# Optimization experiments

Hardware: AMD Instinct MI355X
Metric: run time of the kernel (lower is better)

Reference implementation:

```python
import jax, jax.numpy as jnp
import numpy as np

K = 256  # number of leaf nodes in the cluster tree


def setup_inputs() -> dict:
    key = jax.random.key(0)
    k1, k2 = jax.random.split(key)
    minibatch = jax.random.normal(k1, (131072, 64), dtype=jnp.float32)
    centers = jax.random.normal(k2, (K, 64), dtype=jnp.float32)
    return {"minibatch": minibatch, "centers": centers}


def reference(minibatch, centers):
    # Euclidean cdist (p=2) between samples [N,D] and leaf centers [K,D]
    x_sq = jnp.sum(minibatch * minibatch, axis=1, keepdims=True)      # [N,1]
    c_sq = jnp.sum(centers * centers, axis=1)[None, :]                # [1,K]
    dist_sq = x_sq + c_sq - 2.0 * (minibatch @ centers.T)             # [N,K]
    dist_sq = jnp.maximum(dist_sq, 0.0)
    dist = jnp.sqrt(dist_sq)

    # nearest-leaf routing (torch.min over dim=1)
    assignments = jnp.argmin(dist, axis=1)                            # [N] int
    min_dists = jnp.min(dist, axis=1)                                 # [N]

    # per-leaf statistics (vectorized form of the per-node assignment loop):
    # counts -> node.assignments length, sums -> analytic center updates,
    # sum_sq -> node.sum_squared_dist
    ones = jnp.ones(minibatch.shape[0], dtype=minibatch.dtype)
    leaf_counts = jax.ops.segment_sum(ones, assignments, num_segments=K)           # [K]
    leaf_sums = jax.ops.segment_sum(minibatch, assignments, num_segments=K)        # [K,D]
    leaf_sum_sq_dist = jax.ops.segment_sum(min_dists * min_dists, assignments,
                                           num_segments=K)                         # [K]
    return assignments, min_dists, leaf_counts, leaf_sums, leaf_sum_sq_dist
```

## Files before the change

kernel.cpp:

```cpp
#include <hip/hip_runtime.h>
#include <hip/hip_bf16.h>
#include <float.h>

#define NS 131072
#define DD 64
#define KK 256
#define CPAD 72
#define NSTAT 16896
#define XTS 264
#define XTSW 132
#define NCOPY 512
#define RGROUPS 16
#define RPER 32
#define SCR_OFF_F ((size_t)NCOPY * NSTAT / 2)
#define P_OFF_F   (SCR_OFF_F + (size_t)RGROUPS * NSTAT)
#define P_CSQ_F 9216
#define P_IMG_I4 2304

typedef __attribute__((ext_vector_type(8))) short bf16x8;
typedef __attribute__((ext_vector_type(4))) float f32x4;
typedef __attribute__((ext_vector_type(4))) unsigned int u32x4;


__global__ void zero_buf(float* __restrict__ p, int n) {
    int i = blockIdx.x * 256 + threadIdx.x;
    if (i < n) p[i] = 0.f;
}

__device__ inline unsigned short f2bf(float f) {
    union { __hip_bfloat16 h; unsigned short u; } v;
    v.h = __float2bfloat16(f);
    return v.u;
}
__device__ inline float bf2f(unsigned short b) {
    return __uint_as_float(((unsigned)b) << 16);
}

__global__ void prep_centers(const float* __restrict__ ctr, float* __restrict__ P) {
    __shared__ float s_part[32][9];
    const int t = threadIdx.x;
    const int rl = t >> 3, seg = t & 7;
    const int r = blockIdx.x * 32 + rl;
    const float* rp = ctr + r * DD + seg * 8;
    float4 a = ((const float4*)rp)[0];
    float4 b = ((const float4*)rp)[1];
    unsigned short u0 = f2bf(a.x), u1 = f2bf(a.y), u2 = f2bf(a.z), u3 = f2bf(a.w);
    unsigned short u4 = f2bf(b.x), u5 = f2bf(b.y), u6 = f2bf(b.z), u7 = f2bf(b.w);
    float q0 = bf2f(u0), q1 = bf2f(u1), q2 = bf2f(u2), q3 = bf2f(u3);
    float q4 = bf2f(u4), q5 = bf2f(u5), q6 = bf2f(u6), q7 = bf2f(u7);
    float p = (q0*q0 + q1*q1 + q2*q2 + q3*q3) + (q4*q4 + q5*q5 + q6*q6 + q7*q7);

    unsigned short* Pu = (unsigned short*)P;
    int4 pack;
    pack.x = (int)((unsigned)u0 | ((unsigned)u1 << 16));
    pack.y = (int)((unsigned)u2 | ((unsigned)u3 << 16));
    pack.z = (int)((unsigned)u4 | ((unsigned)u5 << 16));
    pack.w = (int)((unsigned)u6 | ((unsigned)u7 << 16));
    *(int4*)(Pu + (size_t)r * CPAD + seg * 8) = pack;
    if (seg == 0) {
        int4 z; z.x = 0; z.y = 0; z.z = 0; z.w = 0;
        *(int4*)(Pu + (size_t)r * CPAD + 64) = z;
    }
    s_part[rl][seg] = p;
    __syncthreads();
    if (seg == 0) {
        float s = 0.f;
        #pragma unroll
        for (int k = 0; k < 8; ++k) s += s_part[rl][k];
        P[P_CSQ_F + r] = s;
    }
}

__global__ __launch_bounds__(256, 4)
void deepect_argmin(const float* __restrict__ mb, const float* __restrict__ P,
                    float* __restrict__ out) {
    __shared__ __align__(16) unsigned short s_ctr[KK][CPAD];
    __shared__ float s_csq[KK];

    const int tid  = threadIdx.x;
    const int lane = tid & 63;
    const int w    = tid >> 6;
    const int g    = lane >> 4;
    const int c16  = lane & 15;

    {
        const int4* Pi = (const int4*)P;
        int4* Sd = (int4*)s_ctr;
        #pragma unroll
        for (int i = 0; i < 9; ++i)
            Sd[i * 256 + tid] = Pi[i * 256 + tid];
    }
    s_csq[tid] = P[P_CSQ_F + tid];
    __syncthreads();

    float csqh[16];
    #pragma unroll
    for (int t = 0; t < 16; ++t) csqh[t] = -0.5f * s_csq[t * 16 + c16];

    const int sbase = blockIdx.x * 128 + w * 32;

    bf16x8 afr[2][2];
    float  xsq_rt[2];
    #pragma unroll
    for (int rt = 0; rt < 2; ++rt) {
        float px = 0.f;
        #pragma unroll
        for (int ks = 0; ks < 2; ++ks) {
            const float* rp = mb + (size_t)(sbase + rt * 16 + c16) * DD + g * 8 + ks * 32;
            float4 a = ((const float4*)rp)[0];
            float4 b = ((const float4*)rp)[1];
            bf16x8 f;
            f[0] = (short)f2bf(a.x); f[1] = (short)f2bf(a.y);
            f[2] = (short)f2bf(a.z); f[3] = (short)f2bf(a.w);
            f[4] = (short)f2bf(b.x); f[5] = (short)f2bf(b.y);
            f[6] = (short)f2bf(b.z); f[7] = (short)f2bf(b.w);
            afr[rt][ks] = f;
            px += a.x*a.x + a.y*a.y + a.z*a.z + a.w*a.w
                + b.x*b.x + b.y*b.y + b.z*b.z + b.w*b.w;
        }
        px += __shfl_xor(px, 16, 64);
        px += __shfl_xor(px, 32, 64);
        xsq_rt[rt] = px;
    }

    float bestv[2][4];
    int   besti[2][4];
    #pragma unroll
    for (int rt = 0; rt < 2; ++rt)
        #pragma unroll
        for (int r = 0; r < 4; ++r) { bestv[rt][r] = -FLT_MAX; besti[rt][r] = 0; }

    #pragma unroll
    for (int t = 0; t < 16; ++t) {
        const bf16x8 b0 = *(const bf16x8*)&s_ctr[t * 16 + c16][g * 8];
        const bf16x8 b1 = *(const bf16x8*)&s_ctr[t * 16 + c16][g * 8 + 32];
        const int colidx = t * 16 + c16;
        #pragma unroll
        for (int rt = 0; rt < 2; ++rt) {
            f32x4 acc;
            acc[0] = csqh[t]; acc[1] = csqh[t]; acc[2] = csqh[t]; acc[3] = csqh[t];
            acc = __builtin_amdgcn_mfma_f32_16x16x32_bf16(afr[rt][0], b0, acc, 0, 0, 0);
            acc = __builtin_amdgcn_mfma_f32_16x16x32_bf16(afr[rt][1], b1, acc, 0, 0, 0);
            #pragma unroll
            for (int r = 0; r < 4; ++r) {
                if (acc[r] > bestv[rt][r]) { bestv[rt][r] = acc[r]; besti[rt][r] = colidx; }
            }
        }
    }

    float* o_assign = out;
    float* o_mind   = out + NS;

    #pragma unroll
    for (int rt = 0; rt < 2; ++rt) {
        #pragma unroll
        for (int r = 0; r < 4; ++r) {
            float v  = bestv[rt][r];
            int   bi = besti[rt][r];
            #pragma unroll
            for (int off = 1; off < 16; off <<= 1) {
                float ov = __shfl_xor(v, off, 64);
                int   oi = __shfl_xor(bi, off, 64);
                if (ov > v || (ov == v && oi < bi)) { v = ov; bi = oi; }
            }
            int src = (lane & 48) | (g * 4 + r);
            float xq = __shfl(xsq_rt[rt], src, 64);
            float dsq = fmaxf(xq - 2.0f * v, 0.f);
            if (c16 == 0) {
                int s = sbase + rt * 16 + g * 4 + r;
                o_assign[s] = (float)bi;
                o_mind[s]   = sqrtf(dsq);
            }
        }
    }
}

__global__ __launch_bounds__(512, 2)
void deepect_stats_gemm(const float* __restrict__ mb, const float* __restrict__ out,
                        float* __restrict__ ws) {
    __shared__ __align__(16) unsigned short s_xt[80][XTS];
    __shared__ int s_bi[256];

    const int tid  = threadIdx.x;
    const int lane = tid & 63;
    const int w    = tid >> 6;
    const int g    = lane >> 4;
    const int c16  = lane & 15;
    const int base = blockIdx.x * 256;

    unsigned* xtw = (unsigned*)s_xt;

    for (int i = tid; i < 14 * XTSW; i += 512) xtw[66 * XTSW + i] = 0u;

    {
        const int dh = tid >> 7, sp = tid & 127;
        const float* r0 = mb + (size_t)(base + 2 * sp) * DD + dh * 16;
        const float* r1 = r0 + DD;
        #pragma unroll
        for (int q = 0; q < 4; ++q) {
            float4 a = ((const float4*)r0)[q];
            float4 b = ((const float4*)r1)[q];
            const int row = dh * 16 + q * 4;
            xtw[(row + 0) * XTSW + sp] = (unsigned)f2bf(a.x) | ((unsigned)f2bf(b.x) << 16);
            xtw[(row + 1) * XTSW + sp] = (unsigned)f2bf(a.y) | ((unsigned)f2bf(b.y) << 16);
            xtw[(row + 2) * XTSW + sp] = (unsigned)f2bf(a.z) | ((unsigned)f2bf(b.z) << 16);
            xtw[(row + 3) * XTSW + sp] = (unsigned)f2bf(a.w) | ((unsigned)f2bf(b.w) << 16);
        }
    }
    if (tid < 128) {
        const int sp = tid;
        float m0 = out[NS + base + 2 * sp];
        float m1 = out[NS + base + 2 * sp + 1];
        xtw[64 * XTSW + sp] = 0x3F803F80u;
        xtw[65 * XTSW + sp] = (unsigned)f2bf(m0 * m0) | ((unsigned)f2bf(m1 * m1) << 16);
    }
    if (tid < 256) s_bi[tid] = (int)out[base + tid];
    __syncthreads();

    f32x4 acc[2][5];
    #pragma unroll
    for (int L = 0; L < 2; ++L)
        #pragma unroll
        for (int dt = 0; dt < 5; ++dt) {
            acc[L][dt][0] = 0.f; acc[L][dt][1] = 0.f;
            acc[L][dt][2] = 0.f; acc[L][dt][3] = 0.f;
        }

    const int ml0 = w * 16 + c16;
    const int ml1 = (w + 8) * 16 + c16;

    #pragma unroll
    for (int ks = 0; ks < 8; ++ks) {
        const int kb = ks * 32 + g * 8;
        int4 bl = *(int4*)&s_bi[kb];
        int4 bh = *(int4*)&s_bi[kb + 4];
        bf16x8 bfrag[5];
        #pragma unroll
        for (int dt = 0; dt < 5; ++dt)
            bfrag[dt] = *(bf16x8*)&s_xt[dt * 16 + c16][kb];

        const int b0 = bl.x, b1 = bl.y, b2 = bl.z, b3 = bl.w;
        const int b4 = bh.x, b5 = bh.y, b6 = bh.z, b7 = bh.w;
        u32x4 u0, u1;
        u0[0] = (b0 == ml0 ? 0x3F80u : 0u) | (b1 == ml0 ? 0x3F800000u : 0u);
        u0[1] = (b2 == ml0 ? 0x3F80u : 0u) | (b3 == ml0 ? 0x3F800000u : 0u);
        u0[2] = (b4 == ml0 ? 0x3F80u : 0u) | (b5 == ml0 ? 0x3F800000u : 0u);
        u0[3] = (b6 == ml0 ? 0x3F80u : 0u) | (b7 == ml0 ? 0x3F800000u : 0u);
        u1[0] = (b0 == ml1 ? 0x3F80u : 0u) | (b1 == ml1 ? 0x3F800000u : 0u);
        u1[1] = (b2 == ml1 ? 0x3F80u : 0u) | (b3 == ml1 ? 0x3F800000u : 0u);
        u1[2] = (b4 == ml1 ? 0x3F80u : 0u) | (b5 == ml1 ? 0x3F800000u : 0u);
        u1[3] = (b6 == ml1 ? 0x3F80u : 0u) | (b7 == ml1 ? 0x3F800000u : 0u);
        bf16x8 a0 = __builtin_bit_cast(bf16x8, u0);
        bf16x8 a1 = __builtin_bit_cast(bf16x8, u1);

        #pragma unroll
        for (int dt = 0; dt < 5; ++dt) {
            acc[0][dt] = __builtin_amdgcn_mfma_f32_16x16x32_bf16(a0, bfrag[dt], acc[0][dt], 0, 0, 0);
            acc[1][dt] = __builtin_amdgcn_mfma_f32_16x16x32_bf16(a1, bfrag[dt], acc[1][dt], 0, 0, 0);
        }
    }

    unsigned short* dstu = (unsigned short*)ws + (size_t)blockIdx.x * NSTAT;
    #pragma unroll
    for (int L = 0; L < 2; ++L) {
        const int lt = (L == 0) ? w : (w + 8);
        #pragma unroll
        for (int dt = 0; dt < 5; ++dt) {
            const int col = dt * 16 + c16;
            #pragma unroll
            for (int r = 0; r < 4; ++r) {
                const int leaf = lt * 16 + g * 4 + r;
                if (col < 66) dstu[leaf * 66 + col] = f2bf(acc[L][dt][r]);
            }
        }
    }
}

__global__ void reduce_ws1(float* __restrict__ ws) {
    int gid = blockIdx.x * 256 + threadIdx.x;
    if (gid >= NSTAT * RGROUPS) return;
    int g = gid / NSTAT, e = gid - g * NSTAT;
    const unsigned short* src = (const unsigned short*)ws + (size_t)(g * RPER) * NSTAT + e;
    float s = 0.f;
    #pragma unroll 8
    for (int j = 0; j < RPER; ++j) s += bf2f(src[(size_t)j * NSTAT]);
    ws[SCR_OFF_F + (size_t)g * NSTAT + e] = s;
}

__global__ void reduce_ws2(const float* __restrict__ ws, float* __restrict__ o_stats) {
    int e = blockIdx.x * 256 + threadIdx.x;
    if (e >= NSTAT) return;
    float s = 0.f;
    #pragma unroll
    for (int g = 0; g < RGROUPS; ++g) s += ws[SCR_OFF_F + (size_t)g * NSTAT + e];
    int leaf = e / 66, c = e - leaf * 66;
    float* o_cnt = o_stats;
    float* o_sum = o_stats + KK;
    float* o_ssq = o_stats + KK + KK * DD;
    if (c < 64)       o_sum[leaf * 64 + c] = s;
    else if (c == 64) o_cnt[leaf] = s;
    else              o_ssq[leaf] = s;
}

__global__ __launch_bounds__(512, 2)
void deepect_argmin_fb(const float* __restrict__ mb, const float* __restrict__ ctr,
                       float* __restrict__ out) {
    __shared__ __align__(16) unsigned short s_ctr[KK][CPAD];
    __shared__ float s_csq[KK];

    const int tid  = threadIdx.x;
    const int lane = tid & 63;
    const int w    = tid >> 6;
    const int g    = lane >> 4;
    const int c16  = lane & 15;

    for (int idx = tid; idx < KK * 16; idx += 512) {
        int row = idx >> 4, f4 = idx & 15;
        float4 v = ((const float4*)(ctr + row * DD))[f4];
        ushort4 b;
        b.x = f2bf(v.x); b.y = f2bf(v.y); b.z = f2bf(v.z); b.w = f2bf(v.w);
        *(ushort4*)&s_ctr[row][f4 * 4] = b;
    }
    __syncthreads();

    if (tid < KK) {
        float acc = 0.f;
        #pragma unroll
        for (int j = 0; j < 16; ++j) {
            ushort4 b = *(ushort4*)&s_ctr[tid][j * 4];
            float x0 = bf2f(b.x), x1 = bf2f(b.y), x2 = bf2f(b.z), x3 = bf2f(b.w);
            acc += x0 * x0 + x1 * x1 + x2 * x2 + x3 * x3;
        }
        s_csq[tid] = acc;
    }
    __syncthreads();

    float csqh[16];
    #pragma unroll
    for (int t = 0; t < 16; ++t) csqh[t] = -0.5f * s_csq[t * 16 + c16];

    const int sbase = blockIdx.x * 256 + w * 32;

    bf16x8 afr[2][2];
    float  xsq_rt[2];
    #pragma unroll
    for (int rt = 0; rt < 2; ++rt) {
        float px = 0.f;
        #pragma unroll
        for (int ks = 0; ks < 2; ++ks) {
            const float* rp = mb + (size_t)(sbase + rt * 16 + c16) * DD + g * 8 + ks * 32;
            float4 a = ((const float4*)rp)[0];
            float4 b = ((const float4*)rp)[1];
            bf16x8 f;
            f[0] = (short)f2bf(a.x); f[1] = (short)f2bf(a.y);
            f[2] = (short)f2bf(a.z); f[3] = (short)f2bf(a.w);
            f[4] = (short)f2bf(b.x); f[5] = (short)f2bf(b.y);
            f[6] = (short)f2bf(b.z); f[7] = (short)f2bf(b.w);
            afr[rt][ks] = f;
            px += a.x*a.x + a.y*a.y + a.z*a.z + a.w*a.w
                + b.x*b.x + b.y*b.y + b.z*b.z + b.w*b.w;
        }
        px += __shfl_xor(px, 16, 64);
        px += __shfl_xor(px, 32, 64);
        xsq_rt[rt] = px;
    }

    float bestv[2][4];
    int   besti[2][4];
    #pragma unroll
    for (int rt = 0; rt < 2; ++rt)
        #pragma unroll
        for (int r = 0; r < 4; ++r) { bestv[rt][r] = -FLT_MAX; besti[rt][r] = 0; }

    #pragma unroll
    for (int t = 0; t < 16; ++t) {
        bf16x8 b0 = *(bf16x8*)&s_ctr[t * 16 + c16][g * 8];
        bf16x8 b1 = *(bf16x8*)&s_ctr[t * 16 + c16][g * 8 + 32];
        const int colidx = t * 16 + c16;
        #pragma unroll
        for (int rt = 0; rt < 2; ++rt) {
            f32x4 acc;
            acc[0] = csqh[t]; acc[1] = csqh[t]; acc[2] = csqh[t]; acc[3] = csqh[t];
            acc = __builtin_amdgcn_mfma_f32_16x16x32_bf16(afr[rt][0], b0, acc, 0, 0, 0);
            acc = __builtin_amdgcn_mfma_f32_16x16x32_bf16(afr[rt][1], b1, acc, 0, 0, 0);
            #pragma unroll
            for (int r = 0; r < 4; ++r) {
                if (acc[r] > bestv[rt][r]) { bestv[rt][r] = acc[r]; besti[rt][r] = colidx; }
            }
        }
    }

    float* o_assign = out;
    float* o_mind   = out + NS;

    #pragma unroll
    for (int rt = 0; rt < 2; ++rt) {
        #pragma unroll
        for (int r = 0; r < 4; ++r) {
            float v  = bestv[rt][r];
            int   bi = besti[rt][r];
            #pragma unroll
            for (int off = 1; off < 16; off <<= 1) {
                float ov = __shfl_xor(v, off, 64);
                int   oi = __shfl_xor(bi, off, 64);
                if (ov > v || (ov == v && oi < bi)) { v = ov; bi = oi; }
            }
            int src = (lane & 48) | (g * 4 + r);
            float xq = __shfl(xsq_rt[rt], src, 64);
            float dsq = fmaxf(xq - 2.0f * v, 0.f);
            if (c16 == 0) {
                int s = sbase + rt * 16 + g * 4 + r;
                o_assign[s] = (float)bi;
                o_mind[s]   = sqrtf(dsq);
            }
        }
    }
}

__global__ __launch_bounds__(512)
void deepect_stats_atomic(const float* __restrict__ mb, const float* __restrict__ out,
                          float* __restrict__ o_stats) {
    __shared__ float s_cnt[KK];
    __shared__ float s_ssq[KK];
    __shared__ float s_sum[KK][65];

    const int tid = threadIdx.x;
    for (int idx = tid; idx < KK; idx += 512) { s_cnt[idx] = 0.f; s_ssq[idx] = 0.f; }
    for (int idx = tid; idx < KK * 65; idx += 512) ((float*)s_sum)[idx] = 0.f;
    __syncthreads();

    const int grp = tid >> 4;
    const int d4  = tid & 15;
    const int ibase = blockIdx.x * 512 + grp * 16;

    for (int s = 0; s < 16; ++s) {
        const int i = ibase + s;
        const int bi = (int)out[i];
        float4 v = ((const float4*)(mb + (size_t)i * DD))[d4];
        atomicAdd(&s_sum[bi][d4 * 4 + 0], v.x);
        atomicAdd(&s_sum[bi][d4 * 4 + 1], v.y);
        atomicAdd(&s_sum[bi][d4 * 4 + 2], v.z);
        atomicAdd(&s_sum[bi][d4 * 4 + 3], v.w);
        if (d4 == 0) {
            const float md = out[NS + i];
            atomicAdd(&s_cnt[bi], 1.0f);
            atomicAdd(&s_ssq[bi], md * md);
        }
    }
    __syncthreads();

    for (int idx = tid; idx < KK; idx += 512) {
        atomicAdd(&o_stats[idx], s_cnt[idx]);
        atomicAdd(&o_stats[KK + KK * DD + idx], s_ssq[idx]);
    }
    for (int idx = tid; idx < KK * DD; idx += 512)
        atomicAdd(&o_stats[KK + idx], s_sum[idx >> 6][idx & 63]);
}

extern "C" void kernel_launch(void* const* d_in, const int* in_sizes, int n_in,
                              void* d_out, int out_size, void* d_ws, size_t ws_size,
                              hipStream_t stream) {
    const float* mb  = (const float*)d_in[0];
    const float* ctr = (const float*)d_in[1];
    float* out = (float*)d_out;
    float* o_stats = out + 2 * NS;
    float* ws = (float*)d_ws;

    const size_t need = (P_OFF_F + P_CSQ_F + KK) * sizeof(float);

    if (ws_size >= need) {
        float* P = ws + P_OFF_F;
        hipLaunchKernelGGL(prep_centers, dim3(8), dim3(256), 0, stream, ctr, P);
        hipLaunchKernelGGL(deepect_argmin, dim3(NS / 128), dim3(256), 0, stream,
                           mb, P, out);
        hipLaunchKernelGGL(deepect_stats_gemm, dim3(NS / 256), dim3(512), 0, stream,
                           mb, out, ws);
        hipLaunchKernelGGL(reduce_ws1, dim3((NSTAT * RGROUPS + 255) / 256), dim3(256),
                           0, stream, ws);
        hipLaunchKernelGGL(reduce_ws2, dim3((NSTAT + 255) / 256), dim3(256), 0, stream,
                           ws, o_stats);
    } else {
        hipLaunchKernelGGL(zero_buf, dim3((NSTAT + 255) / 256), dim3(256), 0, stream,
                           o_stats, NSTAT);
        hipLaunchKernelGGL(deepect_argmin_fb, dim3(NS / 256), dim3(512), 0, stream,
                           mb, ctr, out);
        hipLaunchKernelGGL(deepect_stats_atomic, dim3(NS / 512), dim3(512), 0, stream,
                           mb, out, o_stats);
    }
}
```

Baseline: 58.45 us.

## Store per-block stats partials in fp32, enlarge argmin blocks, use manual bf16 rounding

The per-block leaf statistics partials return from bf16 to fp32, doubling workspace traffic for the partial-sum reduction. The first reduction pass now writes in place instead of to a separate scratch region. The argmin kernel moves to 512-thread blocks covering 256 samples, and the row norm is computed from bf16-rounded values to match the quantized GEMM. f2bf becomes an integer round-to-nearest-even routine in place of the HIP intrinsic. This mostly trades speed for accuracy and consistency, with extra memory traffic in the stats path.

```diff
diff --git a/kernel.cpp b/kernel.cpp
--- a/kernel.cpp
+++ b/kernel.cpp
@@ -1,5 +1,4 @@
 #include <hip/hip_runtime.h>
-#include <hip/hip_bf16.h>
 #include <float.h>
 
 #define NS 131072
@@ -12,8 +11,7 @@
 #define NCOPY 512
 #define RGROUPS 16
 #define RPER 32
-#define SCR_OFF_F ((size_t)NCOPY * NSTAT / 2)
-#define P_OFF_F   (SCR_OFF_F + (size_t)RGROUPS * NSTAT)
+#define P_OFF_F ((size_t)NCOPY * NSTAT)
 #define P_CSQ_F 9216
 #define P_IMG_I4 2304
 
@@ -28,9 +26,9 @@
 }
 
 __device__ inline unsigned short f2bf(float f) {
-    union { __hip_bfloat16 h; unsigned short u; } v;
-    v.h = __float2bfloat16(f);
-    return v.u;
+    unsigned u = __float_as_uint(f);
+    u += 0x7FFFu + ((u >> 16) & 1u);
+    return (unsigned short)(u >> 16);
 }
 __device__ inline float bf2f(unsigned short b) {
     return __uint_as_float(((unsigned)b) << 16);
@@ -71,7 +69,33 @@
     }
 }
 
-__global__ __launch_bounds__(256, 4)
+__global__ void reduce_ws1(float* __restrict__ ws) {
+    int gid = blockIdx.x * 256 + threadIdx.x;
+    if (gid >= NSTAT * RGROUPS) return;
+    int g = gid / NSTAT, e = gid - g * NSTAT;
+    const float* src = ws + (size_t)(g * RPER) * NSTAT + e;
+    float s = 0.f;
+    #pragma unroll 8
+    for (int j = 0; j < RPER; ++j) s += src[(size_t)j * NSTAT];
+    ws[(size_t)(g * RPER) * NSTAT + e] = s;
+}
+
+__global__ void reduce_ws2(const float* __restrict__ ws, float* __restrict__ o_stats) {
+    int e = blockIdx.x * 256 + threadIdx.x;
+    if (e >= NSTAT) return;
+    float s = 0.f;
+    #pragma unroll
+    for (int g = 0; g < RGROUPS; ++g) s += ws[(size_t)(g * RPER) * NSTAT + e];
+    int leaf = e / 66, c = e - leaf * 66;
+    float* o_cnt = o_stats;
+    float* o_sum = o_stats + KK;
+    float* o_ssq = o_stats + KK + KK * DD;
+    if (c < 64)       o_sum[leaf * 64 + c] = s;
+    else if (c == 64) o_cnt[leaf] = s;
+    else              o_ssq[leaf] = s;
+}
+
+__global__ __launch_bounds__(512, 2)
 void deepect_argmin(const float* __restrict__ mb, const float* __restrict__ P,
                     float* __restrict__ out) {
     __shared__ __align__(16) unsigned short s_ctr[KK][CPAD];
@@ -87,17 +111,19 @@
         const int4* Pi = (const int4*)P;
         int4* Sd = (int4*)s_ctr;
         #pragma unroll
-        for (int i = 0; i < 9; ++i)
-            Sd[i * 256 + tid] = Pi[i * 256 + tid];
-    }
-    s_csq[tid] = P[P_CSQ_F + tid];
+        for (int i = 0; i < 5; ++i) {
+            int idx = i * 512 + tid;
+            if (idx < P_IMG_I4) Sd[idx] = Pi[idx];
+        }
+    }
+    if (tid < KK) s_csq[tid] = P[P_CSQ_F + tid];
     __syncthreads();
 
     float csqh[16];
     #pragma unroll
     for (int t = 0; t < 16; ++t) csqh[t] = -0.5f * s_csq[t * 16 + c16];
 
-    const int sbase = blockIdx.x * 128 + w * 32;
+    const int sbase = blockIdx.x * 256 + w * 32;
 
     bf16x8 afr[2][2];
     float  xsq_rt[2];
@@ -115,8 +141,9 @@
             f[4] = (short)f2bf(b.x); f[5] = (short)f2bf(b.y);
             f[6] = (short)f2bf(b.z); f[7] = (short)f2bf(b.w);
             afr[rt][ks] = f;
-            px += a.x*a.x + a.y*a.y + a.z*a.z + a.w*a.w
-                + b.x*b.x + b.y*b.y + b.z*b.z + b.w*b.w;
+            float q0 = bf2f(f2bf(a.x)), q1 = bf2f(f2bf(a.y)), q2 = bf2f(f2bf(a.z)), q3 = bf2f(f2bf(a.w));
+            float q4 = bf2f(f2bf(b.x)), q5 = bf2f(f2bf(b.y)), q6 = bf2f(f2bf(b.z)), q7 = bf2f(f2bf(b.w));
+            px += q0*q0 + q1*q1 + q2*q2 + q3*q3 + q4*q4 + q5*q5 + q6*q6 + q7*q7;
         }
         px += __shfl_xor(px, 16, 64);
         px += __shfl_xor(px, 32, 64);
@@ -132,8 +159,8 @@
 
     #pragma unroll
     for (int t = 0; t < 16; ++t) {
-        const bf16x8 b0 = *(const bf16x8*)&s_ctr[t * 16 + c16][g * 8];
-        const bf16x8 b1 = *(const bf16x8*)&s_ctr[t * 16 + c16][g * 8 + 32];
+        bf16x8 b0 = *(bf16x8*)&s_ctr[t * 16 + c16][g * 8];
+        bf16x8 b1 = *(bf16x8*)&s_ctr[t * 16 + c16][g * 8 + 32];
         const int colidx = t * 16 + c16;
         #pragma unroll
         for (int rt = 0; rt < 2; ++rt) {
@@ -260,7 +287,7 @@
         }
     }
 
-    unsigned short* dstu = (unsigned short*)ws + (size_t)blockIdx.x * NSTAT;
+    float* dst = ws + (size_t)blockIdx.x * NSTAT;
     #pragma unroll
     for (int L = 0; L < 2; ++L) {
         const int lt = (L == 0) ? w : (w + 8);
@@ -270,36 +297,10 @@
             #pragma unroll
             for (int r = 0; r < 4; ++r) {
                 const int leaf = lt * 16 + g * 4 + r;
-                if (col < 66) dstu[leaf * 66 + col] = f2bf(acc[L][dt][r]);
-            }
-        }
-    }
-}
-
-__global__ void reduce_ws1(float* __restrict__ ws) {
-    int gid = blockIdx.x * 256 + threadIdx.x;
-    if (gid >= NSTAT * RGROUPS) return;
-    int g = gid / NSTAT, e = gid - g * NSTAT;
-    const unsigned short* src = (const unsigned short*)ws + (size_t)(g * RPER) * NSTAT + e;
-    float s = 0.f;
-    #pragma unroll 8
-    for (int j = 0; j < RPER; ++j) s += bf2f(src[(size_t)j * NSTAT]);
-    ws[SCR_OFF_F + (size_t)g * NSTAT + e] = s;
-}
-
-__global__ void reduce_ws2(const float* __restrict__ ws, float* __restrict__ o_stats) {
-    int e = blockIdx.x * 256 + threadIdx.x;
-    if (e >= NSTAT) return;
-    float s = 0.f;
-    #pragma unroll
-    for (int g = 0; g < RGROUPS; ++g) s += ws[SCR_OFF_F + (size_t)g * NSTAT + e];
-    int leaf = e / 66, c = e - leaf * 66;
-    float* o_cnt = o_stats;
-    float* o_sum = o_stats + KK;
-    float* o_ssq = o_stats + KK + KK * DD;
-    if (c < 64)       o_sum[leaf * 64 + c] = s;
-    else if (c == 64) o_cnt[leaf] = s;
-    else              o_ssq[leaf] = s;
+                if (col < 66) dst[leaf * 66 + col] = acc[L][dt][r];
+            }
+        }
+    }
 }
 
 __global__ __launch_bounds__(512, 2)
@@ -357,8 +358,9 @@
             f[4] = (short)f2bf(b.x); f[5] = (short)f2bf(b.y);
             f[6] = (short)f2bf(b.z); f[7] = (short)f2bf(b.w);
             afr[rt][ks] = f;
-            px += a.x*a.x + a.y*a.y + a.z*a.z + a.w*a.w
-                + b.x*b.x + b.y*b.y + b.z*b.z + b.w*b.w;
+            float q0 = bf2f(f2bf(a.x)), q1 = bf2f(f2bf(a.y)), q2 = bf2f(f2bf(a.z)), q3 = bf2f(f2bf(a.w));
+            float q4 = bf2f(f2bf(b.x)), q5 = bf2f(f2bf(b.y)), q6 = bf2f(f2bf(b.z)), q7 = bf2f(f2bf(b.w));
+            px += q0*q0 + q1*q1 + q2*q2 + q3*q3 + q4*q4 + q5*q5 + q6*q6 + q7*q7;
         }
         px += __shfl_xor(px, 16, 64);
         px += __shfl_xor(px, 32, 64);
@@ -471,7 +473,7 @@
     if (ws_size >= need) {
         float* P = ws + P_OFF_F;
         hipLaunchKernelGGL(prep_centers, dim3(8), dim3(256), 0, stream, ctr, P);
-        hipLaunchKernelGGL(deepect_argmin, dim3(NS / 128), dim3(256), 0, stream,
+        hipLaunchKernelGGL(deepect_argmin, dim3(NS / 256), dim3(512), 0, stream,
                            mb, P, out);
         hipLaunchKernelGGL(deepect_stats_gemm, dim3(NS / 256), dim3(512), 0, stream,
                            mb, out, ws);
```

Result: faster. 52.38 us (-10.4%).
